# Kernel tuning notes

Measured on AMD Instinct MI355X. Metric: run time of the kernel, lower is better.

The kernel has to match this reference:

```python
import jax, jax.numpy as jnp
import numpy as np

K = 3            # kernel_size
SCALE = 10.0     # softmax_scale
RES_SCALE = 1.0
CH = 64
RED = 2
CR = CH // RED   # reduced channels = 32


def _unfold(x, k):
    # torch nn.Unfold(kernel_size=k, stride=1): [B,C,H,W] -> [B, C*k*k, L]
    # feature order is channel-major then (kh, kw), matching torch.
    B, C, H, W = x.shape
    Hp, Wp = H - k + 1, W - k + 1
    cols = jnp.stack([x[:, :, di:di + Hp, dj:dj + Wp]
                      for di in range(k) for dj in range(k)], axis=2)  # [B,C,k*k,Hp,Wp]
    return cols.reshape(B, C * k * k, Hp * Wp)


def _fold(p, H, W, k):
    # torch nn.Fold: sum overlapping patches back. p: [B, C*k*k, L1]
    B, Ck2, L = p.shape
    C = Ck2 // (k * k)
    Hp, Wp = H - k + 1, W - k + 1
    p = p.reshape(B, C, k, k, Hp, Wp)
    out = jnp.zeros((B, C, H, W), p.dtype)
    for di in range(k):
        for dj in range(k):
            out = out.at[:, :, di:di + Hp, dj:dj + Wp].add(p[:, :, di, dj])
    return out


def _conv1x1_prelu(x, w, b, a):
    # 1x1 conv + PReLU(single shared slope a)
    y = jnp.einsum('bchw,oc->bohw', x, w) + b[None, :, None, None]
    return jnp.where(y >= 0, y, a * y)


def setup_inputs() -> dict:
    key = jax.random.key(0)
    ks = jax.random.split(key, 7)
    B, C, H, W = 1, CH, 40, 40
    inp = {
        'x':  jax.random.normal(ks[0], (B, C, H, W), jnp.float32),
        'w1': jax.random.normal(ks[1], (CR, CH), jnp.float32) * 0.05,
        'b1': jnp.zeros((CR,), jnp.float32),
        'a1': jnp.asarray(0.25, jnp.float32),
        'w2': jax.random.normal(ks[2], (CR, CH), jnp.float32) * 0.05,
        'b2': jnp.zeros((CR,), jnp.float32),
        'a2': jnp.asarray(0.25, jnp.float32),
        'w3': jax.random.normal(ks[3], (CH, CR), jnp.float32) * 0.05,
        'b3': jnp.zeros((CH,), jnp.float32),
        'a3': jnp.asarray(0.25, jnp.float32),
    }
    return inp


def reference(x, w1, b1, a1, w2, b2, a2, w3, b3, a3):
    B, C, H, W = x.shape
    # conv_match1 + global-max L2 normalization
    base = _conv1x1_prelu(x, w1, b1, a1)                      # [B,CR,H,W]
    base_max = jnp.max(jnp.sqrt(jnp.sum(base ** 2, axis=(1, 2, 3))))
    base_u = _unfold(base, K)                                  # [B, CR*9, L1]
    basen_u = base_u / base_max
    xd = x.reshape(B, C, H // 2, 2, W // 2, 2).mean(axis=(3, 5))
    wf = _conv1x1_prelu(xd, w2, b2, a2)                        # [B,CR,H/2,W/2]
    w_max = jnp.max(jnp.sqrt(jnp.sum(wf ** 2, axis=(1, 2, 3))))
    w_u = _unfold(wf, K)                                       # [B, CR*9, L2]
    wn_u = w_u / w_max
    L1 = base_u.shape[-1]
    # patch tensors [B, CR, 9, L] with L = L1 + L2
    pa = jnp.concatenate([base_u, w_u], -1).reshape(B, CR, K * K, -1)
    pan = jnp.concatenate([basen_u, wn_u], -1).reshape(B, CR, K * K, -1)
    # per-channel patch correlation attention
    yi = jnp.einsum('bckl,bckm->bclm', pan, pan)               # [B,CR,L,L]
    yi = jax.nn.softmax(yi * SCALE, axis=-2)                   # softmax over rows (dim=-2)
    out = jnp.einsum('bckl,bclm->bckm', pa, yi)[..., :L1]      # keep base patches only
    out = out.reshape(B, CR * K * K, L1)
    out = _fold(out, H, W, K) / float(K * K)
    y = _conv1x1_prelu(out, w3, b3, a3)
    return y + RES_SCALE * x
```

## Files before the change

### kernel.cpp

```cpp
#include <hip/hip_runtime.h>

#define L1V 1444
#define CRV 32
#define CHV 64
#define HWV 1600
#define KQ 448
#define NTIL 28
#define ROWH 20
#define NQT 91

typedef float    f32x4 __attribute__((ext_vector_type(4)));
typedef _Float16 f16x4 __attribute__((ext_vector_type(4)));

__global__ __launch_bounds__(256) void k_front(const float* __restrict__ x,
    const float* __restrict__ w1, const float* __restrict__ b1, const float* __restrict__ a1,
    const float* __restrict__ w2, const float* __restrict__ b2, const float* __restrict__ a2,
    float* __restrict__ base, float* __restrict__ wf, float* __restrict__ sumsq)
{
    int t = blockIdx.x * 256 + threadIdx.x;
    float sq = 0.f;
    if (t < CRV * HWV) {
        int c = t / HWV, px = t - c * HWV;
        float acc = b1[c];
        #pragma unroll 8
        for (int ic = 0; ic < CHV; ++ic) acc += w1[c * CHV + ic] * x[ic * HWV + px];
        float a = a1[0];
        float v = acc >= 0.f ? acc : a * acc;
        base[t] = v;
        sq = v * v;
    } else {
        int u = t - CRV * HWV;
        int c = u / 400, p = u - c * 400;
        int i = p / 20, j = p - i * 20;
        int px0 = (2 * i) * 40 + 2 * j;
        float acc = b2[c];
        for (int ic = 0; ic < CHV; ++ic) {
            const float* xp = x + ic * HWV + px0;
            float xd = 0.25f * (xp[0] + xp[1] + xp[40] + xp[41]);
            acc += w2[c * CHV + ic] * xd;
        }
        float a = a2[0];
        float v = acc >= 0.f ? acc : a * acc;
        wf[u] = v;
        sq = v * v;
    }
    __shared__ float red[256];
    red[threadIdx.x] = sq;
    __syncthreads();
    for (int s = 128; s > 0; s >>= 1) {
        if (threadIdx.x < s) red[threadIdx.x] += red[threadIdx.x + s];
        __syncthreads();
    }
    if (threadIdx.x == 0) atomicAdd(&sumsq[blockIdx.x < 200 ? 0 : 1], red[0]);
}

__global__ __launch_bounds__(256, 3) void k_attn(const float* __restrict__ base,
    const float* __restrict__ wf, const float* __restrict__ sumsq,
    float* __restrict__ part)
{
    __shared__ _Float16 panL[KQ * ROWH];
    const int qg   = blockIdx.x;
    const int c    = blockIdx.y;
    const int qtr  = blockIdx.z;
    const int tid  = threadIdx.x;
    const float bmax = sqrtf(sumsq[0]);
    const float wmax = sqrtf(sumsq[1]);
    const float invb = 1.0f / bmax, invw = 1.0f / wmax;
    const float SC = 14.4269504089f;

    for (int s = tid; s < KQ; s += 256) {
        int g = qtr * KQ + s;
        float v[9];
        float one = 0.f;
        if (g < L1V) {
            int i = g / 38, j = g - i * 38;
            const float* src = base + c * HWV + i * 40 + j;
            #pragma unroll
            for (int kh = 0; kh < 3; ++kh)
                #pragma unroll
                for (int kw = 0; kw < 3; ++kw) v[kh * 3 + kw] = src[kh * 40 + kw] * invb;
            one = 1.f;
        } else if (g >= 1456 && g < 1780) {
            int l2 = g - 1456;
            int i = l2 / 18, j = l2 - i * 18;
            const float* src = wf + c * 400 + i * 20 + j;
            #pragma unroll
            for (int kh = 0; kh < 3; ++kh)
                #pragma unroll
                for (int kw = 0; kw < 3; ++kw) v[kh * 3 + kw] = src[kh * 20 + kw] * invw;
            one = 1.f;
        } else {
            #pragma unroll
            for (int k = 0; k < 9; ++k) v[k] = 0.f;
        }
        f16x4 r0, r1, r2a, r3;
        r0[0] = (_Float16)v[0]; r0[1] = (_Float16)v[1]; r0[2] = (_Float16)v[2]; r0[3] = (_Float16)v[3];
        r1[0] = (_Float16)v[4]; r1[1] = (_Float16)v[5]; r1[2] = (_Float16)v[6]; r1[3] = (_Float16)v[7];
        r2a[0] = (_Float16)v[8]; r2a[1] = (_Float16)one; r2a[2] = (_Float16)0.f; r2a[3] = (_Float16)0.f;
        r3 = (f16x4)(_Float16)0.f;
        _Float16* row = &panL[s * ROWH];
        *(f16x4*)&row[0]  = r0;
        *(f16x4*)&row[4]  = r1;
        *(f16x4*)&row[8]  = r2a;
        *(f16x4*)&row[12] = r3;
    }

    const int lane = tid & 63, w = tid >> 6;
    const int g16 = lane >> 4, c16 = lane & 15;
    f16x4 qf[4];
    int qtile[4];
    #pragma unroll
    for (int u = 0; u < 4; ++u) {
        qtile[u] = qg * 16 + w * 4 + u;
        int m = qtile[u] * 16 + c16;
        #pragma unroll
        for (int j = 0; j < 4; ++j) {
            int k = g16 * 4 + j;
            float val = 0.f;
            if (k <= 8 && m < L1V && qtile[u] < NQT) {
                int i = m / 38, jj = m - i * 38;
                val = base[c * HWV + (i + k / 3) * 40 + (jj + k % 3)] * invb * SC;
            }
            qf[u][j] = (_Float16)val;
        }
    }
    __syncthreads();

    f32x4 accB[4] = {{0.f,0.f,0.f,0.f},{0.f,0.f,0.f,0.f},{0.f,0.f,0.f,0.f},{0.f,0.f,0.f,0.f}};
    f32x4 accW[4] = {{0.f,0.f,0.f,0.f},{0.f,0.f,0.f,0.f},{0.f,0.f,0.f,0.f},{0.f,0.f,0.f,0.f}};
    int BT = NQT - qtr * NTIL;
    if (BT < 0) BT = 0;
    if (BT > NTIL) BT = NTIL;

    #define ATTN_TILE(ACC)                                                        \
    {                                                                             \
        const int rb = lt * 16;                                                   \
        f16x4 af = *(const f16x4*)&panL[(rb + c16) * ROWH + g16 * 4];             \
        const int r2 = rb + g16 * 4;                                              \
        f16x4 b2;                                                                 \
        b2[0] = panL[(r2 + 0) * ROWH + c16];                                      \
        b2[1] = panL[(r2 + 1) * ROWH + c16];                                      \
        b2[2] = panL[(r2 + 2) * ROWH + c16];                                      \
        b2[3] = panL[(r2 + 3) * ROWH + c16];                                      \
        _Pragma("unroll")                                                         \
        for (int u = 0; u < 4; ++u) {                                             \
            f32x4 d1 = __builtin_amdgcn_mfma_f32_16x16x16f16(af, qf[u],           \
                           (f32x4){0.f,0.f,0.f,0.f}, 0, 0, 0);                    \
            f16x4 a2;                                                             \
            a2[0] = (_Float16)__builtin_amdgcn_exp2f(d1[0]);                      \
            a2[1] = (_Float16)__builtin_amdgcn_exp2f(d1[1]);                      \
            a2[2] = (_Float16)__builtin_amdgcn_exp2f(d1[2]);                      \
            a2[3] = (_Float16)__builtin_amdgcn_exp2f(d1[3]);                      \
            ACC[u] = __builtin_amdgcn_mfma_f32_16x16x16f16(a2, b2, ACC[u],        \
                                                           0, 0, 0);              \
        }                                                                         \
    }

    for (int lt = 0;  lt < BT;   ++lt) ATTN_TILE(accB)
    for (int lt = BT; lt < NTIL; ++lt) ATTN_TILE(accW)
    #undef ATTN_TILE

    if (c16 < 10) {
        #pragma unroll
        for (int u = 0; u < 4; ++u) {
            if (qtile[u] >= NQT) continue;
            #pragma unroll
            for (int i = 0; i < 4; ++i) {
                int qs = qtile[u] * 16 + g16 * 4 + i;
                if (qs < L1V) {
                    float v = (c16 == 9) ? (accB[u][i] + accW[u][i])
                                         : fmaf(bmax, accB[u][i], wmax * accW[u][i]);
                    part[((size_t)(qtr * CRV + c) * 1536 + qs) * 10 + c16] = v;
                }
            }
        }
    }
}

__global__ __launch_bounds__(256) void k_comb(const float* __restrict__ part,
                                              float* __restrict__ patches)
{
    int t = blockIdx.x * 256 + threadIdx.x;
    if (t >= CRV * L1V) return;
    int c = t / L1V, m = t - c * L1V;
    float tot[10];
    #pragma unroll
    for (int j = 0; j < 10; ++j) tot[j] = 0.f;
    #pragma unroll
    for (int q = 0; q < 4; ++q) {
        const float* p = part + ((size_t)(q * CRV + c) * 1536 + m) * 10;
        #pragma unroll
        for (int j = 0; j < 10; ++j) tot[j] += p[j];
    }
    float inv = 1.0f / tot[9];
    #pragma unroll
    for (int k = 0; k < 9; ++k)
        patches[(c * 9 + k) * L1V + m] = tot[k] * inv;
}

__global__ __launch_bounds__(256) void k_fold(const float* __restrict__ patches,
                                              float* __restrict__ folded)
{
    int t = blockIdx.x * 256 + threadIdx.x;
    if (t >= CRV * HWV) return;
    int c = t / HWV, px = t - c * HWV;
    int h = px / 40, w = px - h * 40;
    float acc = 0.f;
    #pragma unroll
    for (int di = 0; di < 3; ++di) {
        int i = h - di;
        if (i < 0 || i >= 38) continue;
        #pragma unroll
        for (int dj = 0; dj < 3; ++dj) {
            int j = w - dj;
            if (j < 0 || j >= 38) continue;
            acc += patches[(c * 9 + di * 3 + dj) * L1V + i * 38 + j];
        }
    }
    folded[t] = acc * (1.0f / 9.0f);
}

__global__ __launch_bounds__(256) void k_out(const float* __restrict__ folded,
    const float* __restrict__ w3, const float* __restrict__ b3, const float* __restrict__ a3,
    const float* __restrict__ x, float* __restrict__ out)
{
    int t = blockIdx.x * 256 + threadIdx.x;
    if (t >= CHV * HWV) return;
    int oc = t / HWV, px = t - oc * HWV;
    float acc = b3[oc];
    #pragma unroll
    for (int ic = 0; ic < CRV; ++ic) acc += w3[oc * CRV + ic] * folded[ic * HWV + px];
    float a = a3[0];
    float v = acc >= 0.f ? acc : a * acc;
    out[t] = v + x[t];
}

extern "C" void kernel_launch(void* const* d_in, const int* in_sizes, int n_in,
                              void* d_out, int out_size, void* d_ws, size_t ws_size,
                              hipStream_t stream)
{
    const float* x  = (const float*)d_in[0];
    const float* w1 = (const float*)d_in[1];
    const float* b1 = (const float*)d_in[2];
    const float* a1 = (const float*)d_in[3];
    const float* w2 = (const float*)d_in[4];
    const float* b2 = (const float*)d_in[5];
    const float* a2 = (const float*)d_in[6];
    const float* w3 = (const float*)d_in[7];
    const float* b3 = (const float*)d_in[8];
    const float* a3 = (const float*)d_in[9];

    float* ws      = (float*)d_ws;
    float* sumsq   = ws;
    float* base    = ws + 64;
    float* wfb     = base + CRV * HWV;
    float* patches = wfb + 12800;
    float* folded  = patches + CRV * 9 * L1V;
    float* part    = folded + CRV * HWV;

    hipMemsetAsync(sumsq, 0, 2 * sizeof(float), stream);
    k_front<<<250, 256, 0, stream>>>(x, w1, b1, a1, w2, b2, a2, base, wfb, sumsq);
    k_attn<<<dim3(6, CRV, 4), 256, 0, stream>>>(base, wfb, sumsq, part);
    k_comb<<<181, 256, 0, stream>>>(part, patches);
    k_fold<<<200, 256, 0, stream>>>(patches, folded);
    k_out<<<400, 256, 0, stream>>>(folded, w3, b3, a3, x, (float*)d_out);
}
```

Measured before the change: 45.83 us.

## Widen query tiles per wave, prefetch LDS tiles, fuse combine and fold

The attention kernel now handles 6 query tiles per wave instead of 4, which cuts the grid from 6 to 4 query groups. It also software-pipelines the LDS loads of the next key tile ahead of the MFMA/exp compute. The partial-combine and fold kernels are merged into one per-channel kernel that stages normalized patches in shared memory, removing a global round trip and a launch. In exchange, the launch-bounds occupancy target drops from 3 to 2 blocks, the fused kernel uses only 32 blocks with about 52KB of LDS each, and register pressure rises.

```diff
diff --git a/kernel.cpp b/kernel.cpp
--- a/kernel.cpp
+++ b/kernel.cpp
@@ -8,6 +8,7 @@
 #define NTIL 28
 #define ROWH 20
 #define NQT 91
+#define QPW 6
 
 typedef float    f32x4 __attribute__((ext_vector_type(4)));
 typedef _Float16 f16x4 __attribute__((ext_vector_type(4)));
@@ -54,7 +55,7 @@
     if (threadIdx.x == 0) atomicAdd(&sumsq[blockIdx.x < 200 ? 0 : 1], red[0]);
 }
 
-__global__ __launch_bounds__(256, 3) void k_attn(const float* __restrict__ base,
+__global__ __launch_bounds__(256, 2) void k_attn(const float* __restrict__ base,
     const float* __restrict__ wf, const float* __restrict__ sumsq,
     float* __restrict__ part)
 {
@@ -107,11 +108,11 @@
 
     const int lane = tid & 63, w = tid >> 6;
     const int g16 = lane >> 4, c16 = lane & 15;
-    f16x4 qf[4];
-    int qtile[4];
+    f16x4 qf[QPW];
+    int qtile[QPW];
     #pragma unroll
-    for (int u = 0; u < 4; ++u) {
-        qtile[u] = qg * 16 + w * 4 + u;
+    for (int u = 0; u < QPW; ++u) {
+        qtile[u] = qg * 24 + w * QPW + u;
         int m = qtile[u] * 16 + c16;
         #pragma unroll
         for (int j = 0; j < 4; ++j) {
@@ -126,43 +127,59 @@
     }
     __syncthreads();
 
-    f32x4 accB[4] = {{0.f,0.f,0.f,0.f},{0.f,0.f,0.f,0.f},{0.f,0.f,0.f,0.f},{0.f,0.f,0.f,0.f}};
-    f32x4 accW[4] = {{0.f,0.f,0.f,0.f},{0.f,0.f,0.f,0.f},{0.f,0.f,0.f,0.f},{0.f,0.f,0.f,0.f}};
+    f32x4 accB[QPW], accW[QPW];
+    #pragma unroll
+    for (int u = 0; u < QPW; ++u) { accB[u] = (f32x4){0.f,0.f,0.f,0.f}; accW[u] = (f32x4){0.f,0.f,0.f,0.f}; }
     int BT = NQT - qtr * NTIL;
     if (BT < 0) BT = 0;
     if (BT > NTIL) BT = NTIL;
 
-    #define ATTN_TILE(ACC)                                                        \
+    #define LOADT(LT, AF, B2)                                                     \
     {                                                                             \
-        const int rb = lt * 16;                                                   \
-        f16x4 af = *(const f16x4*)&panL[(rb + c16) * ROWH + g16 * 4];             \
-        const int r2 = rb + g16 * 4;                                              \
-        f16x4 b2;                                                                 \
-        b2[0] = panL[(r2 + 0) * ROWH + c16];                                      \
-        b2[1] = panL[(r2 + 1) * ROWH + c16];                                      \
-        b2[2] = panL[(r2 + 2) * ROWH + c16];                                      \
-        b2[3] = panL[(r2 + 3) * ROWH + c16];                                      \
+        const int rb_ = (LT) * 16;                                                \
+        AF = *(const f16x4*)&panL[(rb_ + c16) * ROWH + g16 * 4];                  \
+        const int r2_ = rb_ + g16 * 4;                                            \
+        B2[0] = panL[(r2_ + 0) * ROWH + c16];                                     \
+        B2[1] = panL[(r2_ + 1) * ROWH + c16];                                     \
+        B2[2] = panL[(r2_ + 2) * ROWH + c16];                                     \
+        B2[3] = panL[(r2_ + 3) * ROWH + c16];                                     \
+    }
+
+    #define COMPUTE(ACC, AF, B2)                                                  \
         _Pragma("unroll")                                                         \
-        for (int u = 0; u < 4; ++u) {                                             \
-            f32x4 d1 = __builtin_amdgcn_mfma_f32_16x16x16f16(af, qf[u],           \
+        for (int u = 0; u < QPW; ++u) {                                           \
+            f32x4 d1 = __builtin_amdgcn_mfma_f32_16x16x16f16(AF, qf[u],           \
                            (f32x4){0.f,0.f,0.f,0.f}, 0, 0, 0);                    \
             f16x4 a2;                                                             \
             a2[0] = (_Float16)__builtin_amdgcn_exp2f(d1[0]);                      \
             a2[1] = (_Float16)__builtin_amdgcn_exp2f(d1[1]);                      \
             a2[2] = (_Float16)__builtin_amdgcn_exp2f(d1[2]);                      \
             a2[3] = (_Float16)__builtin_amdgcn_exp2f(d1[3]);                      \
-            ACC[u] = __builtin_amdgcn_mfma_f32_16x16x16f16(a2, b2, ACC[u],        \
+            ACC[u] = __builtin_amdgcn_mfma_f32_16x16x16f16(a2, B2, ACC[u],        \
                                                            0, 0, 0);              \
-        }                                                                         \
-    }
-
-    for (int lt = 0;  lt < BT;   ++lt) ATTN_TILE(accB)
-    for (int lt = BT; lt < NTIL; ++lt) ATTN_TILE(accW)
-    #undef ATTN_TILE
+        }
+
+    f16x4 afC, b2C, afN, b2N;
+    LOADT(0, afC, b2C);
+    int lt = 0;
+    for (; lt < BT; ++lt) {
+        const int nt = (lt + 1 < NTIL) ? lt + 1 : lt;
+        LOADT(nt, afN, b2N);
+        COMPUTE(accB, afC, b2C);
+        afC = afN; b2C = b2N;
+    }
+    for (; lt < NTIL; ++lt) {
+        const int nt = (lt + 1 < NTIL) ? lt + 1 : lt;
+        LOADT(nt, afN, b2N);
+        COMPUTE(accW, afC, b2C);
+        afC = afN; b2C = b2N;
+    }
+    #undef LOADT
+    #undef COMPUTE
 
     if (c16 < 10) {
         #pragma unroll
-        for (int u = 0; u < 4; ++u) {
+        for (int u = 0; u < QPW; ++u) {
             if (qtile[u] >= NQT) continue;
             #pragma unroll
             for (int i = 0; i < 4; ++i) {
@@ -177,47 +194,42 @@
     }
 }
 
-__global__ __launch_bounds__(256) void k_comb(const float* __restrict__ part,
-                                              float* __restrict__ patches)
-{
-    int t = blockIdx.x * 256 + threadIdx.x;
-    if (t >= CRV * L1V) return;
-    int c = t / L1V, m = t - c * L1V;
-    float tot[10];
-    #pragma unroll
-    for (int j = 0; j < 10; ++j) tot[j] = 0.f;
-    #pragma unroll
-    for (int q = 0; q < 4; ++q) {
-        const float* p = part + ((size_t)(q * CRV + c) * 1536 + m) * 10;
-        #pragma unroll
-        for (int j = 0; j < 10; ++j) tot[j] += p[j];
-    }
-    float inv = 1.0f / tot[9];
-    #pragma unroll
-    for (int k = 0; k < 9; ++k)
-        patches[(c * 9 + k) * L1V + m] = tot[k] * inv;
-}
-
-__global__ __launch_bounds__(256) void k_fold(const float* __restrict__ patches,
-                                              float* __restrict__ folded)
-{
-    int t = blockIdx.x * 256 + threadIdx.x;
-    if (t >= CRV * HWV) return;
-    int c = t / HWV, px = t - c * HWV;
-    int h = px / 40, w = px - h * 40;
-    float acc = 0.f;
-    #pragma unroll
-    for (int di = 0; di < 3; ++di) {
-        int i = h - di;
-        if (i < 0 || i >= 38) continue;
-        #pragma unroll
-        for (int dj = 0; dj < 3; ++dj) {
-            int j = w - dj;
-            if (j < 0 || j >= 38) continue;
-            acc += patches[(c * 9 + di * 3 + dj) * L1V + i * 38 + j];
-        }
-    }
-    folded[t] = acc * (1.0f / 9.0f);
+__global__ __launch_bounds__(256) void k_cf(const float* __restrict__ part,
+                                            float* __restrict__ folded)
+{
+    __shared__ float pat[9 * L1V];
+    const int c = blockIdx.x;
+    for (int m = threadIdx.x; m < L1V; m += 256) {
+        float tot[10];
+        #pragma unroll
+        for (int j = 0; j < 10; ++j) tot[j] = 0.f;
+        #pragma unroll
+        for (int q = 0; q < 4; ++q) {
+            const float* p = part + ((size_t)(q * CRV + c) * 1536 + m) * 10;
+            #pragma unroll
+            for (int j = 0; j < 10; ++j) tot[j] += p[j];
+        }
+        float inv = 1.0f / tot[9];
+        #pragma unroll
+        for (int k = 0; k < 9; ++k) pat[k * L1V + m] = tot[k] * inv;
+    }
+    __syncthreads();
+    for (int px = threadIdx.x; px < HWV; px += 256) {
+        int h = px / 40, ww = px - h * 40;
+        float acc = 0.f;
+        #pragma unroll
+        for (int di = 0; di < 3; ++di) {
+            int i = h - di;
+            if (i < 0 || i >= 38) continue;
+            #pragma unroll
+            for (int dj = 0; dj < 3; ++dj) {
+                int j = ww - dj;
+                if (j < 0 || j >= 38) continue;
+                acc += pat[(di * 3 + dj) * L1V + i * 38 + j];
+            }
+        }
+        folded[c * HWV + px] = acc * (1.0f / 9.0f);
+    }
 }
 
 __global__ __launch_bounds__(256) void k_out(const float* __restrict__ folded,
@@ -254,14 +266,12 @@
     float* sumsq   = ws;
     float* base    = ws + 64;
     float* wfb     = base + CRV * HWV;
-    float* patches = wfb + 12800;
-    float* folded  = patches + CRV * 9 * L1V;
+    float* folded  = wfb + 12800;
     float* part    = folded + CRV * HWV;
 
     hipMemsetAsync(sumsq, 0, 2 * sizeof(float), stream);
     k_front<<<250, 256, 0, stream>>>(x, w1, b1, a1, w2, b2, a2, base, wfb, sumsq);
-    k_attn<<<dim3(6, CRV, 4), 256, 0, stream>>>(base, wfb, sumsq, part);
-    k_comb<<<181, 256, 0, stream>>>(part, patches);
-    k_fold<<<200, 256, 0, stream>>>(patches, folded);
+    k_attn<<<dim3(4, CRV, 4), 256, 0, stream>>>(base, wfb, sumsq, part);
+    k_cf<<<CRV, 256, 0, stream>>>(part, folded);
     k_out<<<400, 256, 0, stream>>>(folded, w3, b3, a3, x, (float*)d_out);
 }
```

Result: slower. 48.85 us (+6.6%).
